# Optimization experiments

Measured on AMD Instinct MI355X. Metric: run time of the kernel, lower is better.

The kernel has to match this reference:

```python
import jax, jax.numpy as jnp
import numpy as np


def setup_inputs() -> dict:
    key = jax.random.key(0)
    k = jax.random.split(key, 6)
    B, S, L, V = 512, 256, 128, 32000
    words = jax.random.randint(k[0], (B, S), 0, V)
    encoder_emits = jax.random.normal(k[1], (B, S, L), dtype=jnp.float32)
    mask = jnp.ones((B, S), dtype=bool)  # token 0 always valid; all-valid lengths here
    feature_table = jax.random.normal(k[2], (V, L), dtype=jnp.float32)
    start = jax.random.normal(k[3], (L,), dtype=jnp.float32)
    transitions = jax.random.normal(k[4], (L, L), dtype=jnp.float32)
    end = jax.random.normal(k[5], (L,), dtype=jnp.float32)
    return {"words": words, "encoder_emits": encoder_emits, "mask": mask,
            "feature_table": feature_table, "start": start,
            "transitions": transitions, "end": end}


def reference(words, encoder_emits, mask, feature_table, start, transitions, end):
    # decoder emits: feature_scorer(words) modeled as per-word label-score lookup
    dec = feature_table[words]                       # [B, S, L]
    # init at t = 0
    log_alpha = start[None, :] + encoder_emits[:, 0]  # [B, L]
    log_beta = log_alpha + dec[:, 0]                  # [B, L]

    def step(carry, xs):
        la, lb = carry
        e_i, d_i, m_i = xs                            # [B,L], [B,L], [B]
        crf = e_i[:, None, :] + transitions[None]     # [B, L, L] (prev, cur)
        a_new = jax.nn.logsumexp(la[:, :, None] + crf, axis=1)
        b_new = jax.nn.logsumexp(lb[:, :, None] + crf + d_i[:, None, :], axis=1)
        m = m_i[:, None]
        return (jnp.where(m, a_new, la), jnp.where(m, b_new, lb)), None

    xs = (jnp.swapaxes(encoder_emits[:, 1:], 0, 1),   # [S-1, B, L]
          jnp.swapaxes(dec[:, 1:], 0, 1),
          mask[:, 1:].T)                              # [S-1, B]
    (log_alpha, log_beta), _ = jax.lax.scan(step, (log_alpha, log_beta), xs)

    la = jax.nn.logsumexp(log_alpha + end[None, :], axis=-1)  # [B]
    lb = jax.nn.logsumexp(log_beta + end[None, :], axis=-1)   # [B]
    return (la - lb).sum()
```

## Files before the change

### kernel.cpp

```cpp
#include <hip/hip_runtime.h>


constexpr int SS  = 256;
constexpr int LL  = 128;
constexpr int BB  = 4;
constexpr int BST = 144;

typedef _Float16 half2_t __attribute__((ext_vector_type(2)));
typedef _Float16 half4_t __attribute__((ext_vector_type(4)));
typedef _Float16 half8_t __attribute__((ext_vector_type(8)));
typedef float    f32x4   __attribute__((ext_vector_type(4)));
typedef unsigned uint2_t __attribute__((ext_vector_type(2)));

#define MFMA16(a, b, c) __builtin_amdgcn_mfma_f32_16x16x32_f16((a), (b), (c), 0, 0, 0)
#define PKRTZ(a, b) __builtin_bit_cast(half2_t, __builtin_amdgcn_cvt_pkrtz((a), (b)))

#define BAR() do {                                                \
    asm volatile("s_waitcnt lgkmcnt(0)" ::: "memory");            \
    __builtin_amdgcn_s_barrier();                                 \
    asm volatile("" ::: "memory");                                \
} while (0)

__device__ __forceinline__ float quad_allmax(float x) {
#if __has_builtin(__builtin_amdgcn_permlane16_swap) && __has_builtin(__builtin_amdgcn_permlane32_swap)
    unsigned u = __builtin_bit_cast(unsigned, x);
    uint2_t a = __builtin_amdgcn_permlane16_swap(u, u, false, false);
    float m = fmaxf(__builtin_bit_cast(float, a.x), __builtin_bit_cast(float, a.y));
    unsigned v = __builtin_bit_cast(unsigned, m);
    uint2_t b = __builtin_amdgcn_permlane32_swap(v, v, false, false);
    return fmaxf(__builtin_bit_cast(float, b.x), __builtin_bit_cast(float, b.y));
#else
    x = fmaxf(x, __shfl_xor(x, 16, 64));
    return fmaxf(x, __shfl_xor(x, 32, 64));
#endif
}

__global__ __launch_bounds__(256) void prepass(
    const int* __restrict__ words, const float* __restrict__ emits,
    const float* __restrict__ ftab,
    half4_t* __restrict__ xe, half4_t* __restrict__ xb,
    float* __restrict__ out)
{
    if (blockIdx.x == 0 && threadIdx.x == 0) *out = 0.f;
    const int t = threadIdx.x;
    const int R = blockIdx.x * 8 + (t >> 5);
    const int c = t & 31;
    const int w = words[R];
    const f32x4 e = *(const f32x4*)&emits[(size_t)R * LL + 4 * c];
    const f32x4 d = *(const f32x4*)&ftab[(size_t)w * LL + 4 * c];
    half4_t a, bb;
    #pragma unroll
    for (int r = 0; r < 4; ++r) {
        a[r]  = (_Float16)__expf(e[r]);
        bb[r] = (_Float16)__expf(e[r] + d[r]);
    }
    xe[(size_t)R * 32 + c] = a;
    xb[(size_t)R * 32 + c] = bb;
}

#define STEP(i, XS) do {                                                      \
    const int rp_ = ((i) + 1) & 1, wp_ = (i) & 1;                             \
    O2 -= __log2f(invp);             \
    half8_t bf_[4];                                                           \
    _Pragma("unroll")                                                         \
    for (int c = 0; c < 4; ++c)                                               \
        bf_[c] = *(const half8_t*)&P[rp_][bsl * BST + c * 32 + quad * 8];     \
    f32x4 a_ = MFMA16(areg[0], bf_[0], zero4);                                \
    f32x4 b_ = MFMA16(areg[2], bf_[2], zero4);                                \
    a_ = MFMA16(areg[1], bf_[1], a_);                                         \
    b_ = MFMA16(areg[3], bf_[3], b_);                                         \
    const f32x4 y_ = a_ + b_;                                                 \
    const float p0_ = y_[0] * (float)XS[0] * invp;                            \
    const float p1_ = y_[1] * (float)XS[1] * invp;                            \
    const float p2_ = y_[2] * (float)XS[2] * invp;                            \
    const float p3_ = y_[3] * (float)XS[3] * invp;                            \
    if (m15 < BB) {                                                           \
        half2_t h0_ = PKRTZ(p0_, p1_), h1_ = PKRTZ(p2_, p3_);                 \
        half4_t pa_; pa_[0]=h0_[0]; pa_[1]=h0_[1]; pa_[2]=h1_[0]; pa_[3]=h1_[1];\
        *(half4_t*)&P[wp_][m15 * BST + wave * 16 + col0] = pa_;               \
    }                                                                         \
    const int ipf_ = ((i) + 3 < SS) ? (i) + 3 : SS - 1;                       \
    XS = *(const half4_t*)&X[xrow + (size_t)ipf_ * LL + wave * 16 + col0];    \
    float mm_ = fmaxf(fmaxf(p0_, p1_), fmaxf(p2_, p3_));                      \
    mm_ = quad_allmax(mm_);                                                   \
    if (quad == 0 && m15 < BB) PM[wp_][m15][wave] = mm_;                      \
    BAR();                                                                    \
    const f32x4 pmA_ = *(const f32x4*)&PM[wp_][bsl][0];                       \
    const f32x4 pmB_ = *(const f32x4*)&PM[wp_][bsl][4];                       \
    invp = __builtin_amdgcn_rcpf(                                             \
        fmaxf(fmaxf(fmaxf(pmA_[0], pmA_[1]), fmaxf(pmA_[2], pmA_[3])),        \
              fmaxf(fmaxf(pmB_[0], pmB_[1]), fmaxf(pmB_[2], pmB_[3]))));      \
} while (0)

__global__ __launch_bounds__(512, 1) void crf_scan(
    const float* __restrict__ start,
    const float* __restrict__ trans,
    const float* __restrict__ endv,
    const _Float16* __restrict__ xe,
    const _Float16* __restrict__ xb,
    float* __restrict__ out)
{
    const int blk   = blockIdx.x;
    const int chain = blk & 1;
    const int grp   = blk >> 1;
    const int tid   = threadIdx.x;
    const int wave  = tid >> 6;
    const int lane  = tid & 63;
    const int m15   = lane & 15;
    const int bsl   = m15 & (BB - 1);
    const int quad  = lane >> 4;
    const int col0  = quad * 4;
    const int batch = grp * BB + bsl;
    const _Float16* __restrict__ X = chain ? xb : xe;

    __shared__ __align__(16) _Float16 P[2][BB * BST];
    __shared__ __align__(16) float    PM[2][BB][8];

    half8_t areg[4];
    #pragma unroll
    for (int c = 0; c < 4; ++c)
        #pragma unroll
        for (int jj = 0; jj < 8; ++jj)
            areg[c][jj] = (_Float16)__expf(
                trans[(c * 32 + quad * 8 + jj) * LL + wave * 16 + m15]);

    const size_t xrow = (size_t)batch * SS * LL;
    const f32x4 zero4 = (f32x4){0.f, 0.f, 0.f, 0.f};

    float invp, O2 = 0.f;

    {
        const int s0 = wave * 16 + col0;
        const f32x4  sv = *(const f32x4*)&start[s0];
        const half4_t x0 = *(const half4_t*)&X[xrow + s0];
        float y0 = __expf(sv[0]) * (float)x0[0];
        float y1 = __expf(sv[1]) * (float)x0[1];
        float y2 = __expf(sv[2]) * (float)x0[2];
        float y3 = __expf(sv[3]) * (float)x0[3];
        if (m15 < BB) {
            half2_t h0 = PKRTZ(y0, y1), h1 = PKRTZ(y2, y3);
            half4_t pa; pa[0]=h0[0]; pa[1]=h0[1]; pa[2]=h1[0]; pa[3]=h1[1];
            *(half4_t*)&P[0][m15 * BST + s0] = pa;
        }
        float mm = fmaxf(fmaxf(y0, y1), fmaxf(y2, y3));
        mm = quad_allmax(mm);
        if (quad == 0 && m15 < BB) PM[0][m15][wave] = mm;
    }
    BAR();
    {
        const f32x4 pmA = *(const f32x4*)&PM[0][bsl][0];
        const f32x4 pmB = *(const f32x4*)&PM[0][bsl][4];
        invp = __builtin_amdgcn_rcpf(
            fmaxf(fmaxf(fmaxf(pmA[0], pmA[1]), fmaxf(pmA[2], pmA[3])),
                  fmaxf(fmaxf(pmB[0], pmB[1]), fmaxf(pmB[2], pmB[3]))));
    }

    half4_t xA, xB, xC;
    xA = *(const half4_t*)&X[xrow + (size_t)1 * LL + wave * 16 + col0];
    xB = *(const half4_t*)&X[xrow + (size_t)2 * LL + wave * 16 + col0];
    xC = *(const half4_t*)&X[xrow + (size_t)3 * LL + wave * 16 + col0];

    for (int i = 1; i + 2 < SS; i += 3) {
        STEP(i,     xA);
        STEP(i + 1, xB);
        STEP(i + 2, xC);
    }

    if (wave == 0) {
        float s = 0.f;
        #pragma unroll
        for (int t = 0; t < 8; ++t) {
            const half4_t p  = *(const half4_t*)&P[1][bsl * BST + t * 16 + col0];
            const f32x4   ev = *(const f32x4*)&endv[t * 16 + col0];
            #pragma unroll
            for (int r = 0; r < 4; ++r)
                s += (float)p[r] * __expf(ev[r]);
        }
        s += __shfl_xor(s, 16, 64);
        s += __shfl_xor(s, 32, 64);
        float lf = O2 * 0.6931471805599453f + __logf(s);
        if (chain) lf = -lf;
        if (quad == 0) {
            lf += __shfl_xor(lf, 1, 64);
            lf += __shfl_xor(lf, 2, 64);
            if (m15 == 0) atomicAdd(out, lf);
        }
    }
}

extern "C" void kernel_launch(void* const* d_in, const int* in_sizes, int n_in,
                              void* d_out, int out_size, void* d_ws, size_t ws_size,
                              hipStream_t stream) {
    const int*   words = (const int*)d_in[0];
    const float* emits = (const float*)d_in[1];
    const float* ftab  = (const float*)d_in[3];
    const float* start = (const float*)d_in[4];
    const float* trans = (const float*)d_in[5];
    const float* endv  = (const float*)d_in[6];
    float* out = (float*)d_out;

    half4_t* xe = (half4_t*)d_ws;
    half4_t* xb = xe + (size_t)512 * SS * 32;

    prepass<<<512 * SS / 8, 256, 0, stream>>>(words, emits, ftab, xe, xb, out);
    crf_scan<<<256, 512, 0, stream>>>(start, trans, endv,
                                      (const _Float16*)xe, (const _Float16*)xb, out);
}
```

Baseline: 221.0 us.

## Interleave alpha and beta chains in one block sharing per-step barriers

```diff
diff --git a/kernel.cpp b/kernel.cpp
--- a/kernel.cpp
+++ b/kernel.cpp
@@ -3,7 +3,7 @@
 
 constexpr int SS  = 256;
 constexpr int LL  = 128;
-constexpr int BB  = 4;
+constexpr int BB  = 2;
 constexpr int BST = 144;
 
 typedef _Float16 half2_t __attribute__((ext_vector_type(2)));
@@ -58,38 +58,53 @@
     xb[(size_t)R * 32 + c] = bb;
 }
 
-#define STEP(i, XS) do {                                                      \
-    const int rp_ = ((i) + 1) & 1, wp_ = (i) & 1;                             \
-    O2 -= __log2f(invp);             \
-    half8_t bf_[4];                                                           \
-    _Pragma("unroll")                                                         \
-    for (int c = 0; c < 4; ++c)                                               \
-        bf_[c] = *(const half8_t*)&P[rp_][bsl * BST + c * 32 + quad * 8];     \
-    f32x4 a_ = MFMA16(areg[0], bf_[0], zero4);                                \
-    f32x4 b_ = MFMA16(areg[2], bf_[2], zero4);                                \
-    a_ = MFMA16(areg[1], bf_[1], a_);                                         \
-    b_ = MFMA16(areg[3], bf_[3], b_);                                         \
+#define CHAIN_BODY(PBUF, PMBUF, BF, XS, INVP, O2V, XPTR) do {                 \
+    O2V -= __log2f(INVP);                                                     \
+    f32x4 a_ = MFMA16(areg[0], BF[0], zero4);                                 \
+    f32x4 b_ = MFMA16(areg[2], BF[2], zero4);                                 \
+    a_ = MFMA16(areg[1], BF[1], a_);                                          \
+    b_ = MFMA16(areg[3], BF[3], b_);                                          \
     const f32x4 y_ = a_ + b_;                                                 \
-    const float p0_ = y_[0] * (float)XS[0] * invp;                            \
-    const float p1_ = y_[1] * (float)XS[1] * invp;                            \
-    const float p2_ = y_[2] * (float)XS[2] * invp;                            \
-    const float p3_ = y_[3] * (float)XS[3] * invp;                            \
+    const float p0_ = y_[0] * (float)XS[0] * INVP;                            \
+    const float p1_ = y_[1] * (float)XS[1] * INVP;                            \
+    const float p2_ = y_[2] * (float)XS[2] * INVP;                            \
+    const float p3_ = y_[3] * (float)XS[3] * INVP;                            \
     if (m15 < BB) {                                                           \
         half2_t h0_ = PKRTZ(p0_, p1_), h1_ = PKRTZ(p2_, p3_);                 \
         half4_t pa_; pa_[0]=h0_[0]; pa_[1]=h0_[1]; pa_[2]=h1_[0]; pa_[3]=h1_[1];\
-        *(half4_t*)&P[wp_][m15 * BST + wave * 16 + col0] = pa_;               \
+        *(half4_t*)&PBUF[wp_][m15 * BST + wave * 16 + col0] = pa_;            \
     }                                                                         \
-    const int ipf_ = ((i) + 3 < SS) ? (i) + 3 : SS - 1;                       \
-    XS = *(const half4_t*)&X[xrow + (size_t)ipf_ * LL + wave * 16 + col0];    \
+    XS = *(const half4_t*)&XPTR[xrow + (size_t)ipf_ * LL + wave * 16 + col0]; \
     float mm_ = fmaxf(fmaxf(p0_, p1_), fmaxf(p2_, p3_));                      \
     mm_ = quad_allmax(mm_);                                                   \
-    if (quad == 0 && m15 < BB) PM[wp_][m15][wave] = mm_;                      \
+    if (quad == 0 && m15 < BB) PMBUF[wp_][m15][wave] = mm_;                   \
+} while (0)
+
+#define STEP2(i, XSA, XSB) do {                                               \
+    const int rp_ = ((i) + 1) & 1, wp_ = (i) & 1;                             \
+    const int ipf_ = ((i) + 3 < SS) ? (i) + 3 : SS - 1;                       \
+    half8_t bfA_[4], bfB_[4];                                                 \
+    _Pragma("unroll")                                                         \
+    for (int c = 0; c < 4; ++c)                                               \
+        bfA_[c] = *(const half8_t*)&PA[rp_][bsl * BST + c * 32 + quad * 8];   \
+    _Pragma("unroll")                                                         \
+    for (int c = 0; c < 4; ++c)                                               \
+        bfB_[c] = *(const half8_t*)&PB[rp_][bsl * BST + c * 32 + quad * 8];   \
+    CHAIN_BODY(PA, PMA, bfA_, XSA, invpA, O2A, XE);                           \
+    CHAIN_BODY(PB, PMB, bfB_, XSB, invpB, O2B, XB);                           \
     BAR();                                                                    \
-    const f32x4 pmA_ = *(const f32x4*)&PM[wp_][bsl][0];                       \
-    const f32x4 pmB_ = *(const f32x4*)&PM[wp_][bsl][4];                       \
-    invp = __builtin_amdgcn_rcpf(                                             \
-        fmaxf(fmaxf(fmaxf(pmA_[0], pmA_[1]), fmaxf(pmA_[2], pmA_[3])),        \
-              fmaxf(fmaxf(pmB_[0], pmB_[1]), fmaxf(pmB_[2], pmB_[3]))));      \
+    {                                                                         \
+        const f32x4 mA0 = *(const f32x4*)&PMA[wp_][bsl][0];                   \
+        const f32x4 mA1 = *(const f32x4*)&PMA[wp_][bsl][4];                   \
+        invpA = __builtin_amdgcn_rcpf(                                        \
+            fmaxf(fmaxf(fmaxf(mA0[0], mA0[1]), fmaxf(mA0[2], mA0[3])),        \
+                  fmaxf(fmaxf(mA1[0], mA1[1]), fmaxf(mA1[2], mA1[3]))));      \
+        const f32x4 mB0 = *(const f32x4*)&PMB[wp_][bsl][0];                   \
+        const f32x4 mB1 = *(const f32x4*)&PMB[wp_][bsl][4];                   \
+        invpB = __builtin_amdgcn_rcpf(                                        \
+            fmaxf(fmaxf(fmaxf(mB0[0], mB0[1]), fmaxf(mB0[2], mB0[3])),        \
+                  fmaxf(fmaxf(mB1[0], mB1[1]), fmaxf(mB1[2], mB1[3]))));      \
+    }                                                                         \
 } while (0)
 
 __global__ __launch_bounds__(512, 1) void crf_scan(
@@ -101,8 +116,6 @@
     float* __restrict__ out)
 {
     const int blk   = blockIdx.x;
-    const int chain = blk & 1;
-    const int grp   = blk >> 1;
     const int tid   = threadIdx.x;
     const int wave  = tid >> 6;
     const int lane  = tid & 63;
@@ -110,11 +123,14 @@
     const int bsl   = m15 & (BB - 1);
     const int quad  = lane >> 4;
     const int col0  = quad * 4;
-    const int batch = grp * BB + bsl;
-    const _Float16* __restrict__ X = chain ? xb : xe;
-
-    __shared__ __align__(16) _Float16 P[2][BB * BST];
-    __shared__ __align__(16) float    PM[2][BB][8];
+    const int batch = blk * BB + bsl;
+    const _Float16* __restrict__ XE = xe;
+    const _Float16* __restrict__ XB = xb;
+
+    __shared__ __align__(16) _Float16 PA[2][BB * BST];
+    __shared__ __align__(16) _Float16 PB[2][BB * BST];
+    __shared__ __align__(16) float    PMA[2][BB][8];
+    __shared__ __align__(16) float    PMB[2][BB][8];
 
     half8_t areg[4];
     #pragma unroll
@@ -127,50 +143,71 @@
     const size_t xrow = (size_t)batch * SS * LL;
     const f32x4 zero4 = (f32x4){0.f, 0.f, 0.f, 0.f};
 
-    float invp, O2 = 0.f;
+    float invpA, invpB, O2A = 0.f, O2B = 0.f;
 
     {
         const int s0 = wave * 16 + col0;
-        const f32x4  sv = *(const f32x4*)&start[s0];
-        const half4_t x0 = *(const half4_t*)&X[xrow + s0];
-        float y0 = __expf(sv[0]) * (float)x0[0];
-        float y1 = __expf(sv[1]) * (float)x0[1];
-        float y2 = __expf(sv[2]) * (float)x0[2];
-        float y3 = __expf(sv[3]) * (float)x0[3];
+        const f32x4 sv = *(const f32x4*)&start[s0];
+        float es[4];
+        #pragma unroll
+        for (int r = 0; r < 4; ++r) es[r] = __expf(sv[r]);
+
+        const half4_t xa0 = *(const half4_t*)&XE[xrow + s0];
+        const half4_t xb0 = *(const half4_t*)&XB[xrow + s0];
+        float ya[4], yb[4];
+        #pragma unroll
+        for (int r = 0; r < 4; ++r) {
+            ya[r] = es[r] * (float)xa0[r];
+            yb[r] = es[r] * (float)xb0[r];
+        }
         if (m15 < BB) {
-            half2_t h0 = PKRTZ(y0, y1), h1 = PKRTZ(y2, y3);
+            half2_t h0 = PKRTZ(ya[0], ya[1]), h1 = PKRTZ(ya[2], ya[3]);
             half4_t pa; pa[0]=h0[0]; pa[1]=h0[1]; pa[2]=h1[0]; pa[3]=h1[1];
-            *(half4_t*)&P[0][m15 * BST + s0] = pa;
+            *(half4_t*)&PA[0][m15 * BST + s0] = pa;
+            half2_t g0 = PKRTZ(yb[0], yb[1]), g1 = PKRTZ(yb[2], yb[3]);
+            half4_t pb; pb[0]=g0[0]; pb[1]=g0[1]; pb[2]=g1[0]; pb[3]=g1[1];
+            *(half4_t*)&PB[0][m15 * BST + s0] = pb;
         }
-        float mm = fmaxf(fmaxf(y0, y1), fmaxf(y2, y3));
-        mm = quad_allmax(mm);
-        if (quad == 0 && m15 < BB) PM[0][m15][wave] = mm;
+        float ma = fmaxf(fmaxf(ya[0], ya[1]), fmaxf(ya[2], ya[3]));
+        float mb = fmaxf(fmaxf(yb[0], yb[1]), fmaxf(yb[2], yb[3]));
+        ma = quad_allmax(ma);
+        mb = quad_allmax(mb);
+        if (quad == 0 && m15 < BB) { PMA[0][m15][wave] = ma; PMB[0][m15][wave] = mb; }
     }
     BAR();
     {
-        const f32x4 pmA = *(const f32x4*)&PM[0][bsl][0];
-        const f32x4 pmB = *(const f32x4*)&PM[0][bsl][4];
-        invp = __builtin_amdgcn_rcpf(
-            fmaxf(fmaxf(fmaxf(pmA[0], pmA[1]), fmaxf(pmA[2], pmA[3])),
-                  fmaxf(fmaxf(pmB[0], pmB[1]), fmaxf(pmB[2], pmB[3]))));
-    }
-
-    half4_t xA, xB, xC;
-    xA = *(const half4_t*)&X[xrow + (size_t)1 * LL + wave * 16 + col0];
-    xB = *(const half4_t*)&X[xrow + (size_t)2 * LL + wave * 16 + col0];
-    xC = *(const half4_t*)&X[xrow + (size_t)3 * LL + wave * 16 + col0];
+        const f32x4 mA0 = *(const f32x4*)&PMA[0][bsl][0];
+        const f32x4 mA1 = *(const f32x4*)&PMA[0][bsl][4];
+        invpA = __builtin_amdgcn_rcpf(
+            fmaxf(fmaxf(fmaxf(mA0[0], mA0[1]), fmaxf(mA0[2], mA0[3])),
+                  fmaxf(fmaxf(mA1[0], mA1[1]), fmaxf(mA1[2], mA1[3]))));
+        const f32x4 mB0 = *(const f32x4*)&PMB[0][bsl][0];
+        const f32x4 mB1 = *(const f32x4*)&PMB[0][bsl][4];
+        invpB = __builtin_amdgcn_rcpf(
+            fmaxf(fmaxf(fmaxf(mB0[0], mB0[1]), fmaxf(mB0[2], mB0[3])),
+                  fmaxf(fmaxf(mB1[0], mB1[1]), fmaxf(mB1[2], mB1[3]))));
+    }
+
+    half4_t aS0, aS1, aS2, bS0, bS1, bS2;
+    aS0 = *(const half4_t*)&XE[xrow + (size_t)1 * LL + wave * 16 + col0];
+    aS1 = *(const half4_t*)&XE[xrow + (size_t)2 * LL + wave * 16 + col0];
+    aS2 = *(const half4_t*)&XE[xrow + (size_t)3 * LL + wave * 16 + col0];
+    bS0 = *(const half4_t*)&XB[xrow + (size_t)1 * LL + wave * 16 + col0];
+    bS1 = *(const half4_t*)&XB[xrow + (size_t)2 * LL + wave * 16 + col0];
+    bS2 = *(const half4_t*)&XB[xrow + (size_t)3 * LL + wave * 16 + col0];
 
     for (int i = 1; i + 2 < SS; i += 3) {
-        STEP(i,     xA);
-        STEP(i + 1, xB);
-        STEP(i + 2, xC);
-    }
-
-    if (wave == 0) {
+        STEP2(i,     aS0, bS0);
+        STEP2(i + 1, aS1, bS1);
+        STEP2(i + 2, aS2, bS2);
+    }
+
+    if (wave < 2) {
+        const _Float16* __restrict__ Pf = (wave == 0) ? &PA[1][0] : &PB[1][0];
         float s = 0.f;
         #pragma unroll
         for (int t = 0; t < 8; ++t) {
-            const half4_t p  = *(const half4_t*)&P[1][bsl * BST + t * 16 + col0];
+            const half4_t p  = *(const half4_t*)&Pf[bsl * BST + t * 16 + col0];
             const f32x4   ev = *(const f32x4*)&endv[t * 16 + col0];
             #pragma unroll
             for (int r = 0; r < 4; ++r)
@@ -178,13 +215,11 @@
         }
         s += __shfl_xor(s, 16, 64);
         s += __shfl_xor(s, 32, 64);
-        float lf = O2 * 0.6931471805599453f + __logf(s);
-        if (chain) lf = -lf;
-        if (quad == 0) {
-            lf += __shfl_xor(lf, 1, 64);
-            lf += __shfl_xor(lf, 2, 64);
-            if (m15 == 0) atomicAdd(out, lf);
-        }
+        const float O2v = (wave == 0) ? O2A : O2B;
+        float lf = O2v * 0.6931471805599453f + __logf(s);
+        if (wave == 1) lf = -lf;
+        lf += __shfl_xor(lf, 1, 64);
+        if (lane == 0) atomicAdd(out, lf);
     }
 }
 
```

Measured after the change: 281.4 us. 1.27x slower.
